# Optimization experiments

Hardware: AMD Instinct MI355X
Metric: run time of the kernel (lower is better)

The kernel has to match this reference:

```python
import jax, jax.numpy as jnp
import numpy as np

# SMPL-X mesh sizes; BVH padded collision-pair count P = F * max_collisions
B, NV, F, MAXC = 16, 10475, 20908, 8
P = F * MAXC
SIGMA = 0.001          # distance-field cone height (df_cone_height)
LINEAR_MAX = 1000.0    # linear cap on penetration depth
PENALIZE_OUTSIDE = True  # module config: DistanceFieldPenetrationLoss(penalize_outside=True)


def setup_inputs() -> dict:
    key = jax.random.key(0)
    k1, k2, k3, k4 = jax.random.split(key, 4)
    # body-model output vertices (B, NV, 3)
    v = jax.random.normal(k1, (B, NV, 3), dtype=jnp.float32) * 0.5
    # triangle vertex indices (F, 3)
    faces = jax.random.randint(k2, (F, 3), 0, NV, dtype=jnp.int64)
    # BVH output: padded (intruder, receiver) triangle-index pairs per batch elem,
    # -1 marks invalid (padding) slots, as torch-mesh-isect's BVH emits.
    collision_idxs = jax.random.randint(k3, (B, P, 2), 0, F, dtype=jnp.int64)
    invalid = jax.random.uniform(k4, (B, P, 1)) < 0.75
    collision_idxs = jnp.where(invalid, jnp.int64(-1), collision_idxs)
    return {"v": v, "faces": faces, "collision_idxs": collision_idxs}


def pen_distance(triangles, collision_idxs):
    """Distance-field penetration loss over collision pairs.

    triangles: (B, F, 3, 3); collision_idxs: (B, P, 2) with -1 = invalid pair.
    Returns per-batch loss (B,).
    """
    mask = jnp.all(collision_idxs >= 0, axis=-1)          # (B, P)
    idx = jnp.maximum(collision_idxs, 0)
    # gather intruding / receiving triangles: (B, P, 3, 3)
    intr = jnp.take_along_axis(triangles, idx[..., 0][:, :, None, None], axis=1)
    recv = jnp.take_along_axis(triangles, idx[..., 1][:, :, None, None], axis=1)

    # receiver conic distance field: centroid + unit normal
    c = recv.mean(axis=-2)                                 # (B, P, 3)
    n = jnp.cross(recv[..., 1, :] - recv[..., 0, :],
                  recv[..., 2, :] - recv[..., 0, :])
    n = n / (jnp.linalg.norm(n, axis=-1, keepdims=True) + 1e-12)

    u = intr - c[..., None, :]                             # (B, P, 3v, 3c)
    # signed penetration depth of each intruder vertex (positive = behind plane)
    t = -jnp.einsum('bpvc,bpc->bpv', u, n)                 # (B, P, 3)
    depth = jnp.clip(t, 0.0, LINEAR_MAX)

    if not PENALIZE_OUTSIDE:
        # radial attenuation inside a cone of height SIGMA over the triangle
        radial = jnp.linalg.norm(u + t[..., None] * n[..., None, :], axis=-1)
        r_base = jnp.linalg.norm(recv - c[..., None, :], axis=-1).max(axis=-1)
        cone_r = r_base[..., None] * jnp.clip(1.0 - t / SIGMA, 0.0, 1.0)
        depth = depth * jax.nn.relu(1.0 - radial / (cone_r + 1e-12))

    psi2 = jnp.sum(depth * depth, axis=-1)                 # (B, P)
    return jnp.sum(jnp.where(mask, psi2, 0.0), axis=-1)   # (B,)


def reference(v, faces, collision_idxs):
    # triangles = v.view(-1,3)[faces_ids] : per-batch triangle vertex gather
    triangles = v[:, faces]                                # (B, F, 3, 3)
    # BVH search ran under torch.no_grad(); indices are constants here
    collision_idxs = jax.lax.stop_gradient(collision_idxs)
    return pen_distance(triangles, collision_idxs)
```

## Files before the change

### kernel.cpp

```cpp
#include <hip/hip_runtime.h>

constexpr int B_  = 16;
constexpr int NV_ = 10475;
constexpr int F_  = 20908;
constexpr int P_  = F_ * 8;
constexpr float LINEAR_MAX_ = 1000.0f;

constexpr int REC_PB_  = 82;
constexpr int PAIR_PB_ = 164;
constexpr int QSTRIDE_ = PAIR_PB_ * 256;


__device__ __forceinline__ void swz(int bid, int& b, int& px) {
    const int xcd = bid & 7;
    const int j   = bid >> 3;
    b  = xcd + ((j & 1) << 3);
    px = j >> 1;
}

__global__ __launch_bounds__(256) void face_rec_kernel(
    const float* __restrict__ v,
    const int*   __restrict__ faces,
    float4*      __restrict__ tbl)
{
    __shared__ float4 lds4[1024];

    int b, px; swz(blockIdx.x, b, px);
    const int t  = threadIdx.x;
    const int f0 = px * 256;
    const int f  = f0 + t;
    const int fc = (f < F_) ? f : 0;

    const float* __restrict__ vb = v + (size_t)b * (NV_ * 3);
    const int i0 = faces[fc * 3 + 0] * 3;
    const int i1 = faces[fc * 3 + 1] * 3;
    const int i2 = faces[fc * 3 + 2] * 3;

    const float v0x = vb[i0 + 0], v0y = vb[i0 + 1], v0z = vb[i0 + 2];
    const float v1x = vb[i1 + 0], v1y = vb[i1 + 1], v1z = vb[i1 + 2];
    const float v2x = vb[i2 + 0], v2y = vb[i2 + 1], v2z = vb[i2 + 2];

    const float third = 1.0f / 3.0f;
    const float cx = (v0x + v1x + v2x) * third;
    const float cy = (v0y + v1y + v2y) * third;
    const float cz = (v0z + v1z + v2z) * third;

    const float e1x = v1x - v0x, e1y = v1y - v0y, e1z = v1z - v0z;
    const float e2x = v2x - v0x, e2y = v2y - v0y, e2z = v2z - v0z;
    float nx = e1y * e2z - e1z * e2y;
    float ny = e1z * e2x - e1x * e2z;
    float nz = e1x * e2y - e1y * e2x;
    const float inv = 1.0f / (sqrtf(nx * nx + ny * ny + nz * nz) + 1e-12f);
    nx *= inv; ny *= inv; nz *= inv;

    lds4[t * 4 + 0] = make_float4(nx, ny, nz, cx * nx + cy * ny + cz * nz);
    lds4[t * 4 + 1] = make_float4(v0x, v0y, v0z, v1x);
    lds4[t * 4 + 2] = make_float4(v1y, v1z, v2x, v2y);
    lds4[t * 4 + 3] = make_float4(v2z, 0.0f, 0.0f, 0.0f);
    __syncthreads();

    const int vrec  = F_ - f0;
    const int limit = ((vrec < 256) ? vrec : 256) * 4;
    float4* dst = tbl + ((size_t)b * F_ + f0) * 4;
    #pragma unroll
    for (int j = 0; j < 4; ++j) {
        const int e = j * 256 + t;
        if (e < limit) dst[e] = lds4[e];
    }
}

__global__ __launch_bounds__(256) void pen_pairs_kernel(
    const int2*   __restrict__ coll,
    const float4* __restrict__ tbl,
    float*        __restrict__ part)
{
    int b, px; swz(blockIdx.x, b, px);
    const int p0 = px * 256 + threadIdx.x;

    const int2*   __restrict__ cb = coll + (size_t)b * P_;
    const float4* __restrict__ bt = tbl + (size_t)b * F_ * 4;

    float psi2 = 0.0f;

    #pragma unroll
    for (int k = 0; k < 4; ++k) {
        const int p = p0 + k * QSTRIDE_;
        if (p < P_) {
            const int2 pr = cb[p];
            const float m = ((pr.x | pr.y) >= 0) ? 1.0f : 0.0f;
            const int fR = (pr.y > 0) ? pr.y : 0;
            const int fI = (pr.x > 0) ? pr.x : 0;

            const float4 nd = bt[fR * 4 + 0];
            const float4 L0 = bt[fI * 4 + 1];
            const float4 L1 = bt[fI * 4 + 2];
            const float4 L2 = bt[fI * 4 + 3];

            float s = 0.0f;
            float t0 = nd.w - (L0.x * nd.x + L0.y * nd.y + L0.z * nd.z);
            t0 = fminf(fmaxf(t0, 0.0f), LINEAR_MAX_);
            s = fmaf(t0, t0, s);
            float t1 = nd.w - (L0.w * nd.x + L1.x * nd.y + L1.y * nd.z);
            t1 = fminf(fmaxf(t1, 0.0f), LINEAR_MAX_);
            s = fmaf(t1, t1, s);
            float t2 = nd.w - (L1.z * nd.x + L1.w * nd.y + L2.x * nd.z);
            t2 = fminf(fmaxf(t2, 0.0f), LINEAR_MAX_);
            s = fmaf(t2, t2, s);

            psi2 = fmaf(m, s, psi2);
        }
    }

    #pragma unroll
    for (int off = 32; off > 0; off >>= 1)
        psi2 += __shfl_down(psi2, off, 64);

    __shared__ float wsum[4];
    const int lane = threadIdx.x & 63;
    const int wid  = threadIdx.x >> 6;
    if (lane == 0) wsum[wid] = psi2;
    __syncthreads();

    if (threadIdx.x == 0)
        part[b * PAIR_PB_ + px] = wsum[0] + wsum[1] + wsum[2] + wsum[3];
}

__global__ __launch_bounds__(256) void final_reduce_kernel(
    const float* __restrict__ part,
    float*       __restrict__ out)
{
    const int b = blockIdx.x;
    const int t = threadIdx.x;

    float s = (t < PAIR_PB_) ? part[b * PAIR_PB_ + t] : 0.0f;

    #pragma unroll
    for (int off = 32; off > 0; off >>= 1)
        s += __shfl_down(s, off, 64);

    __shared__ float wsum[4];
    if ((t & 63) == 0) wsum[t >> 6] = s;
    __syncthreads();

    if (t == 0) out[b] = wsum[0] + wsum[1] + wsum[2] + wsum[3];
}

extern "C" void kernel_launch(void* const* d_in, const int* in_sizes, int n_in,
                              void* d_out, int out_size, void* d_ws, size_t ws_size,
                              hipStream_t stream) {
    const float* v     = (const float*)d_in[0];
    const int*   faces = (const int*)d_in[1];
    const int2*  coll  = (const int2*)d_in[2];
    float* out  = (float*)d_out;

    float4* tbl  = (float4*)d_ws;
    float*  part = (float*)((char*)d_ws + (size_t)B_ * F_ * 64);

    dim3 block(256);
    face_rec_kernel   <<<dim3(16 * REC_PB_),  block, 0, stream>>>(v, faces, tbl);
    pen_pairs_kernel  <<<dim3(16 * PAIR_PB_), block, 0, stream>>>(coll, tbl, part);
    final_reduce_kernel<<<dim3(B_),           block, 0, stream>>>(part, out);
}
```

Measured before the change: 92.92 us.

## Pre-pack vertices and faces to float4/int4, load two collision pairs per int4

Adds a pre-pass kernel that repacks vertices into padded float4 and face indices into int4, so the face-record kernel can gather each vertex with one 16-byte load instead of three scalar loads. The pair kernel now reads two collision pairs per int4 load with contiguous per-block chunks and half as many blocks. The cost is an extra kernel launch and extra workspace writes and reads for the packed arrays. The final reduce block shrinks to 128 threads to match the smaller partial count.

```diff
diff --git a/kernel.cpp b/kernel.cpp
--- a/kernel.cpp
+++ b/kernel.cpp
@@ -6,9 +6,9 @@
 constexpr int P_  = F_ * 8;
 constexpr float LINEAR_MAX_ = 1000.0f;
 
+constexpr int VP_PB_   = 41;
 constexpr int REC_PB_  = 82;
-constexpr int PAIR_PB_ = 164;
-constexpr int QSTRIDE_ = PAIR_PB_ * 256;
+constexpr int PAIR_PB_ = 82;
 
 
 __device__ __forceinline__ void swz(int bid, int& b, int& px) {
@@ -18,10 +18,31 @@
     px = j >> 1;
 }
 
-__global__ __launch_bounds__(256) void face_rec_kernel(
+__global__ __launch_bounds__(256) void pre_pack_kernel(
     const float* __restrict__ v,
     const int*   __restrict__ faces,
-    float4*      __restrict__ tbl)
+    float4*      __restrict__ vpack,
+    int4*        __restrict__ faces4)
+{
+    const int bid = blockIdx.x;
+    int b, px; swz(bid, b, px);
+    const int t = threadIdx.x;
+
+    const int g = bid * 256 + t;
+    if (g < F_)
+        faces4[g] = make_int4(faces[g*3+0], faces[g*3+1], faces[g*3+2], 0);
+
+    const int vid = px * 256 + t;
+    if (vid < NV_) {
+        const float* src = v + ((size_t)b * NV_ + vid) * 3;
+        vpack[(size_t)b * NV_ + vid] = make_float4(src[0], src[1], src[2], 0.0f);
+    }
+}
+
+__global__ __launch_bounds__(256) void face_rec_kernel(
+    const float4* __restrict__ vpack,
+    const int4*   __restrict__ faces4,
+    float4*       __restrict__ tbl)
 {
     __shared__ float4 lds4[1024];
 
@@ -31,22 +52,19 @@
     const int f  = f0 + t;
     const int fc = (f < F_) ? f : 0;
 
-    const float* __restrict__ vb = v + (size_t)b * (NV_ * 3);
-    const int i0 = faces[fc * 3 + 0] * 3;
-    const int i1 = faces[fc * 3 + 1] * 3;
-    const int i2 = faces[fc * 3 + 2] * 3;
-
-    const float v0x = vb[i0 + 0], v0y = vb[i0 + 1], v0z = vb[i0 + 2];
-    const float v1x = vb[i1 + 0], v1y = vb[i1 + 1], v1z = vb[i1 + 2];
-    const float v2x = vb[i2 + 0], v2y = vb[i2 + 1], v2z = vb[i2 + 2];
+    const int4 fi = faces4[fc];
+    const float4* __restrict__ vb = vpack + (size_t)b * NV_;
+    const float4 p0 = vb[fi.x];
+    const float4 p1 = vb[fi.y];
+    const float4 p2 = vb[fi.z];
 
     const float third = 1.0f / 3.0f;
-    const float cx = (v0x + v1x + v2x) * third;
-    const float cy = (v0y + v1y + v2y) * third;
-    const float cz = (v0z + v1z + v2z) * third;
+    const float cx = (p0.x + p1.x + p2.x) * third;
+    const float cy = (p0.y + p1.y + p2.y) * third;
+    const float cz = (p0.z + p1.z + p2.z) * third;
 
-    const float e1x = v1x - v0x, e1y = v1y - v0y, e1z = v1z - v0z;
-    const float e2x = v2x - v0x, e2y = v2y - v0y, e2z = v2z - v0z;
+    const float e1x = p1.x - p0.x, e1y = p1.y - p0.y, e1z = p1.z - p0.z;
+    const float e2x = p2.x - p0.x, e2y = p2.y - p0.y, e2z = p2.z - p0.z;
     float nx = e1y * e2z - e1z * e2y;
     float ny = e1z * e2x - e1x * e2z;
     float nz = e1x * e2y - e1y * e2x;
@@ -54,9 +72,9 @@
     nx *= inv; ny *= inv; nz *= inv;
 
     lds4[t * 4 + 0] = make_float4(nx, ny, nz, cx * nx + cy * ny + cz * nz);
-    lds4[t * 4 + 1] = make_float4(v0x, v0y, v0z, v1x);
-    lds4[t * 4 + 2] = make_float4(v1y, v1z, v2x, v2y);
-    lds4[t * 4 + 3] = make_float4(v2z, 0.0f, 0.0f, 0.0f);
+    lds4[t * 4 + 1] = make_float4(p0.x, p0.y, p0.z, p1.x);
+    lds4[t * 4 + 2] = make_float4(p1.y, p1.z, p2.x, p2.y);
+    lds4[t * 4 + 3] = make_float4(p2.z, 0.0f, 0.0f, 0.0f);
     __syncthreads();
 
     const int vrec  = F_ - f0;
@@ -70,44 +88,51 @@
 }
 
 __global__ __launch_bounds__(256) void pen_pairs_kernel(
-    const int2*   __restrict__ coll,
+    const int*    __restrict__ coll,
     const float4* __restrict__ tbl,
     float*        __restrict__ part)
 {
     int b, px; swz(blockIdx.x, b, px);
-    const int p0 = px * 256 + threadIdx.x;
+    const int t = threadIdx.x;
 
-    const int2*   __restrict__ cb = coll + (size_t)b * P_;
+    const int4*   __restrict__ c4 = (const int4*)(coll + (size_t)b * P_ * 2);
     const float4* __restrict__ bt = tbl + (size_t)b * F_ * 4;
 
     float psi2 = 0.0f;
+    const int ibase = px * 1024;
 
     #pragma unroll
     for (int k = 0; k < 4; ++k) {
-        const int p = p0 + k * QSTRIDE_;
-        if (p < P_) {
-            const int2 pr = cb[p];
-            const float m = ((pr.x | pr.y) >= 0) ? 1.0f : 0.0f;
-            const int fR = (pr.y > 0) ? pr.y : 0;
-            const int fI = (pr.x > 0) ? pr.x : 0;
+        const int idx = ibase + (k << 8) + t;
+        if (idx < (P_ >> 1)) {
+            const int4 pp = c4[idx];
 
-            const float4 nd = bt[fR * 4 + 0];
-            const float4 L0 = bt[fI * 4 + 1];
-            const float4 L1 = bt[fI * 4 + 2];
-            const float4 L2 = bt[fI * 4 + 3];
+            #pragma unroll
+            for (int h = 0; h < 2; ++h) {
+                const int ix = (h == 0) ? pp.x : pp.z;
+                const int iy = (h == 0) ? pp.y : pp.w;
+                const float m = ((ix | iy) >= 0) ? 1.0f : 0.0f;
+                const int fR = (iy > 0) ? iy : 0;
+                const int fI = (ix > 0) ? ix : 0;
 
-            float s = 0.0f;
-            float t0 = nd.w - (L0.x * nd.x + L0.y * nd.y + L0.z * nd.z);
-            t0 = fminf(fmaxf(t0, 0.0f), LINEAR_MAX_);
-            s = fmaf(t0, t0, s);
-            float t1 = nd.w - (L0.w * nd.x + L1.x * nd.y + L1.y * nd.z);
-            t1 = fminf(fmaxf(t1, 0.0f), LINEAR_MAX_);
-            s = fmaf(t1, t1, s);
-            float t2 = nd.w - (L1.z * nd.x + L1.w * nd.y + L2.x * nd.z);
-            t2 = fminf(fmaxf(t2, 0.0f), LINEAR_MAX_);
-            s = fmaf(t2, t2, s);
+                const float4 nd = bt[fR * 4 + 0];
+                const float4 L0 = bt[fI * 4 + 1];
+                const float4 L1 = bt[fI * 4 + 2];
+                const float4 L2 = bt[fI * 4 + 3];
 
-            psi2 = fmaf(m, s, psi2);
+                float s = 0.0f;
+                float t0 = nd.w - (L0.x * nd.x + L0.y * nd.y + L0.z * nd.z);
+                t0 = fminf(fmaxf(t0, 0.0f), LINEAR_MAX_);
+                s = fmaf(t0, t0, s);
+                float t1 = nd.w - (L0.w * nd.x + L1.x * nd.y + L1.y * nd.z);
+                t1 = fminf(fmaxf(t1, 0.0f), LINEAR_MAX_);
+                s = fmaf(t1, t1, s);
+                float t2 = nd.w - (L1.z * nd.x + L1.w * nd.y + L2.x * nd.z);
+                t2 = fminf(fmaxf(t2, 0.0f), LINEAR_MAX_);
+                s = fmaf(t2, t2, s);
+
+                psi2 = fmaf(m, s, psi2);
+            }
         }
     }
 
@@ -116,16 +141,16 @@
         psi2 += __shfl_down(psi2, off, 64);
 
     __shared__ float wsum[4];
-    const int lane = threadIdx.x & 63;
-    const int wid  = threadIdx.x >> 6;
+    const int lane = t & 63;
+    const int wid  = t >> 6;
     if (lane == 0) wsum[wid] = psi2;
     __syncthreads();
 
-    if (threadIdx.x == 0)
+    if (t == 0)
         part[b * PAIR_PB_ + px] = wsum[0] + wsum[1] + wsum[2] + wsum[3];
 }
 
-__global__ __launch_bounds__(256) void final_reduce_kernel(
+__global__ __launch_bounds__(128) void final_reduce_kernel(
     const float* __restrict__ part,
     float*       __restrict__ out)
 {
@@ -138,11 +163,11 @@
     for (int off = 32; off > 0; off >>= 1)
         s += __shfl_down(s, off, 64);
 
-    __shared__ float wsum[4];
+    __shared__ float wsum[2];
     if ((t & 63) == 0) wsum[t >> 6] = s;
     __syncthreads();
 
-    if (t == 0) out[b] = wsum[0] + wsum[1] + wsum[2] + wsum[3];
+    if (t == 0) out[b] = wsum[0] + wsum[1];
 }
 
 extern "C" void kernel_launch(void* const* d_in, const int* in_sizes, int n_in,
@@ -150,14 +175,18 @@
                               hipStream_t stream) {
     const float* v     = (const float*)d_in[0];
     const int*   faces = (const int*)d_in[1];
-    const int2*  coll  = (const int2*)d_in[2];
-    float* out  = (float*)d_out;
+    const int*   coll  = (const int*)d_in[2];
+    float* out = (float*)d_out;
 
-    float4* tbl  = (float4*)d_ws;
-    float*  part = (float*)((char*)d_ws + (size_t)B_ * F_ * 64);
+    char* ws = (char*)d_ws;
+    float4* tbl    = (float4*)ws;   ws += (size_t)B_ * F_ * 64;
+    float4* vpack  = (float4*)ws;   ws += (size_t)B_ * NV_ * 16;
+    int4*   faces4 = (int4*)ws;     ws += (size_t)F_ * 16;
+    float*  part   = (float*)ws;
 
     dim3 block(256);
-    face_rec_kernel   <<<dim3(16 * REC_PB_),  block, 0, stream>>>(v, faces, tbl);
+    pre_pack_kernel   <<<dim3(16 * VP_PB_),   block, 0, stream>>>(v, faces, vpack, faces4);
+    face_rec_kernel   <<<dim3(16 * REC_PB_),  block, 0, stream>>>(vpack, faces4, tbl);
     pen_pairs_kernel  <<<dim3(16 * PAIR_PB_), block, 0, stream>>>(coll, tbl, part);
-    final_reduce_kernel<<<dim3(B_),           block, 0, stream>>>(part, out);
+    final_reduce_kernel<<<dim3(B_), dim3(128), 0, stream>>>(part, out);
 }
```

Result: slower. 95.68 us (+3.0%).

## Fuse final reduction into pair kernel via last-block atomic ticket; pad LDS stride

Applied to the files above, without the earlier changes.

Removes the separate final_reduce kernel launch. Each pair block now publishes its partial with a release store and bumps a per-batch atomic counter, and the last block to arrive reduces all partials and writes the output. The counter is reset inside face_rec_kernel. The face-record LDS staging stride also changes from 4 to 5 float4 per thread, meant to cut bank conflicts. This adds atomics and a conditional tail in exchange for one fewer launch.

```diff
diff --git a/kernel.cpp b/kernel.cpp
--- a/kernel.cpp
+++ b/kernel.cpp
@@ -21,12 +21,16 @@
 __global__ __launch_bounds__(256) void face_rec_kernel(
     const float* __restrict__ v,
     const int*   __restrict__ faces,
-    float4*      __restrict__ tbl)
+    float4*      __restrict__ tbl,
+    int*         __restrict__ tick)
 {
-    __shared__ float4 lds4[1024];
+    __shared__ float4 lds4[256 * 5];
 
     int b, px; swz(blockIdx.x, b, px);
     const int t  = threadIdx.x;
+
+    if (blockIdx.x == 0 && t < B_) tick[t] = 0;
+
     const int f0 = px * 256;
     const int f  = f0 + t;
     const int fc = (f < F_) ? f : 0;
@@ -53,10 +57,10 @@
     const float inv = 1.0f / (sqrtf(nx * nx + ny * ny + nz * nz) + 1e-12f);
     nx *= inv; ny *= inv; nz *= inv;
 
-    lds4[t * 4 + 0] = make_float4(nx, ny, nz, cx * nx + cy * ny + cz * nz);
-    lds4[t * 4 + 1] = make_float4(v0x, v0y, v0z, v1x);
-    lds4[t * 4 + 2] = make_float4(v1y, v1z, v2x, v2y);
-    lds4[t * 4 + 3] = make_float4(v2z, 0.0f, 0.0f, 0.0f);
+    lds4[t * 5 + 0] = make_float4(nx, ny, nz, cx * nx + cy * ny + cz * nz);
+    lds4[t * 5 + 1] = make_float4(v0x, v0y, v0z, v1x);
+    lds4[t * 5 + 2] = make_float4(v1y, v1z, v2x, v2y);
+    lds4[t * 5 + 3] = make_float4(v2z, 0.0f, 0.0f, 0.0f);
     __syncthreads();
 
     const int vrec  = F_ - f0;
@@ -65,17 +69,20 @@
     #pragma unroll
     for (int j = 0; j < 4; ++j) {
         const int e = j * 256 + t;
-        if (e < limit) dst[e] = lds4[e];
+        if (e < limit) dst[e] = lds4[(e >> 2) * 5 + (e & 3)];
     }
 }
 
 __global__ __launch_bounds__(256) void pen_pairs_kernel(
     const int2*   __restrict__ coll,
     const float4* __restrict__ tbl,
-    float*        __restrict__ part)
+    float*        __restrict__ part,
+    int*          __restrict__ tick,
+    float*        __restrict__ out)
 {
     int b, px; swz(blockIdx.x, b, px);
-    const int p0 = px * 256 + threadIdx.x;
+    const int t = threadIdx.x;
+    const int p0 = px * 256 + t;
 
     const int2*   __restrict__ cb = coll + (size_t)b * P_;
     const float4* __restrict__ bt = tbl + (size_t)b * F_ * 4;
@@ -116,33 +123,36 @@
         psi2 += __shfl_down(psi2, off, 64);
 
     __shared__ float wsum[4];
-    const int lane = threadIdx.x & 63;
-    const int wid  = threadIdx.x >> 6;
-    if (lane == 0) wsum[wid] = psi2;
+    __shared__ int   lastflag;
+    if ((t & 63) == 0) wsum[t >> 6] = psi2;
     __syncthreads();
 
-    if (threadIdx.x == 0)
-        part[b * PAIR_PB_ + px] = wsum[0] + wsum[1] + wsum[2] + wsum[3];
-}
-
-__global__ __launch_bounds__(256) void final_reduce_kernel(
-    const float* __restrict__ part,
-    float*       __restrict__ out)
-{
-    const int b = blockIdx.x;
-    const int t = threadIdx.x;
-
-    float s = (t < PAIR_PB_) ? part[b * PAIR_PB_ + t] : 0.0f;
-
-    #pragma unroll
-    for (int off = 32; off > 0; off >>= 1)
-        s += __shfl_down(s, off, 64);
-
-    __shared__ float wsum[4];
-    if ((t & 63) == 0) wsum[t >> 6] = s;
+    if (t == 0) {
+        const float blocksum = wsum[0] + wsum[1] + wsum[2] + wsum[3];
+        __hip_atomic_store(&part[b * PAIR_PB_ + px], blocksum,
+                           __ATOMIC_RELEASE, __HIP_MEMORY_SCOPE_AGENT);
+        const int prev = __hip_atomic_fetch_add(&tick[b], 1,
+                           __ATOMIC_ACQ_REL, __HIP_MEMORY_SCOPE_AGENT);
+        lastflag = (prev == PAIR_PB_ - 1);
+    }
     __syncthreads();
 
-    if (t == 0) out[b] = wsum[0] + wsum[1] + wsum[2] + wsum[3];
+    if (lastflag) {
+        float s = 0.0f;
+        if (t < PAIR_PB_)
+            s = __hip_atomic_load(&part[b * PAIR_PB_ + t],
+                                  __ATOMIC_ACQUIRE, __HIP_MEMORY_SCOPE_AGENT);
+
+        #pragma unroll
+        for (int off = 32; off > 0; off >>= 1)
+            s += __shfl_down(s, off, 64);
+
+        __syncthreads();
+        if ((t & 63) == 0) wsum[t >> 6] = s;
+        __syncthreads();
+
+        if (t == 0) out[b] = wsum[0] + wsum[1] + wsum[2] + wsum[3];
+    }
 }
 
 extern "C" void kernel_launch(void* const* d_in, const int* in_sizes, int n_in,
@@ -151,13 +161,14 @@
     const float* v     = (const float*)d_in[0];
     const int*   faces = (const int*)d_in[1];
     const int2*  coll  = (const int2*)d_in[2];
-    float* out  = (float*)d_out;
+    float* out = (float*)d_out;
 
-    float4* tbl  = (float4*)d_ws;
-    float*  part = (float*)((char*)d_ws + (size_t)B_ * F_ * 64);
+    char* ws = (char*)d_ws;
+    float4* tbl  = (float4*)ws;   ws += (size_t)B_ * F_ * 64;
+    float*  part = (float*)ws;    ws += (size_t)B_ * PAIR_PB_ * sizeof(float);
+    int*    tick = (int*)ws;
 
     dim3 block(256);
-    face_rec_kernel   <<<dim3(16 * REC_PB_),  block, 0, stream>>>(v, faces, tbl);
-    pen_pairs_kernel  <<<dim3(16 * PAIR_PB_), block, 0, stream>>>(coll, tbl, part);
-    final_reduce_kernel<<<dim3(B_),           block, 0, stream>>>(part, out);
+    face_rec_kernel <<<dim3(16 * REC_PB_),  block, 0, stream>>>(v, faces, tbl, tick);
+    pen_pairs_kernel<<<dim3(16 * PAIR_PB_), block, 0, stream>>>(coll, tbl, part, tick, out);
 }
```

Result: slower. 170.9 us (+84.0%).
